# Performance work log

Measured on AMD Instinct MI355X. Metric: run time of the kernel, lower is better.

The kernel has to match this reference:

```python
import jax, jax.numpy as jnp
import numpy as np

N_NODES = 100000


def gcn_conv(x, edge_index, W, b):
    """PyG GCNConv: h = x @ W; out = D^-1/2 (A+I) D^-1/2 h + b."""
    n = x.shape[0]
    src, dst = edge_index[0], edge_index[1]
    loop = jnp.arange(n)
    src = jnp.concatenate([src, loop])  # add self-loops
    dst = jnp.concatenate([dst, loop])
    # degree at target nodes (unit edge weights)
    deg = jax.ops.segment_sum(jnp.ones(dst.shape[0], dtype=x.dtype), dst, num_segments=n)
    dinv = jnp.where(deg > 0, jax.lax.rsqrt(deg), 0.0)
    norm = dinv[src] * dinv[dst]  # [E+n]
    h = x @ W  # [n, out]
    msg = h[src] * norm[:, None]  # gather + scale
    out = jax.ops.segment_sum(msg, dst, num_segments=n)  # scatter-add
    return out + b


def setup_inputs() -> dict:
    key = jax.random.key(0)
    k1, k2, k3, k4, k5, k6 = jax.random.split(key, 6)
    E = 3200000
    x = jax.random.normal(k1, (N_NODES, 2), dtype=jnp.float32)
    edge_index = jax.random.randint(k2, (2, E), 0, N_NODES, dtype=jnp.int64)
    W1 = jax.random.normal(k3, (2, 16), dtype=jnp.float32) * 0.5
    b1 = jax.random.normal(k4, (16,), dtype=jnp.float32) * 0.1
    W2 = jax.random.normal(k5, (16, 2), dtype=jnp.float32) * 0.25
    b2 = jax.random.normal(k6, (2,), dtype=jnp.float32) * 0.1
    return {"x": x, "edge_index": edge_index, "W1": W1, "b1": b1, "W2": W2, "b2": b2}


def reference(x, edge_index, W1, b1, W2, b2):
    h = jax.nn.relu(gcn_conv(x, edge_index, W1, b1))
    # dropout is identity at inference
    out = gcn_conv(h, edge_index, W2, b2)
    return jax.nn.log_softmax(out, axis=1)
```

## Files before the change

### kernel.cpp

```cpp
#include <hip/hip_runtime.h>
#include <math.h>


constexpr int N = 100000;
constexpr int LOGB = 6;
constexpr int BNODES = 1 << LOGB;
constexpr int K = (N + BNODES - 1) / BNODES;
constexpr int KF = 49 * 32;
constexpr int CAPF = 2560;
constexpr int NC = 49;
constexpr int CAP1 = 68608;
constexpr int BSP = 512;
constexpr int ECHUNK = 8192;
constexpr int EPT = ECHUNK / BSP;
constexpr int MAXCH = 9;
constexpr int BAGG = 256;

__global__ __launch_bounds__(BSP) void k_pass1(const int* __restrict__ src,
                                               const int* __restrict__ dst, int E,
                                               int* __restrict__ gfill1,
                                               int* __restrict__ slotsC) {
    __shared__ int hist[NC];
    __shared__ int base[NC];
    int t = threadIdx.x;
    if (t < NC) hist[t] = 0;
    __syncthreads();
    int s[EPT], d[EPT];
    int ebase = blockIdx.x * ECHUNK + t * EPT;
#pragma unroll
    for (int k = 0; k < EPT / 4; k++) {
        int idx = ebase + 4 * k;
        if (idx + 3 < E) {
            *(int4*)(s + 4 * k) = *(const int4*)(src + idx);
            *(int4*)(d + 4 * k) = *(const int4*)(dst + idx);
        } else {
            for (int j = 0; j < 4; j++) {
                s[4 * k + j] = (idx + j < E) ? src[idx + j] : -1;
                d[4 * k + j] = (idx + j < E) ? dst[idx + j] : -1;
            }
        }
    }
#pragma unroll
    for (int k = 0; k < EPT; k++)
        if (d[k] >= 0) atomicAdd(&hist[d[k] >> 11], 1);
    __syncthreads();
    if (t < NC) {
        int c = hist[t];
        base[t] = c ? atomicAdd(&gfill1[t], c) : 0;
        hist[t] = 0;
    }
    __syncthreads();
#pragma unroll
    for (int k = 0; k < EPT; k++) {
        if (d[k] >= 0) {
            int bin = d[k] >> 11;
            int r = atomicAdd(&hist[bin], 1);
            int pos = base[bin] + r;
            if (pos < CAP1) slotsC[bin * CAP1 + pos] = (s[k] << 11) | (d[k] & 2047);
        }
    }
}

__global__ __launch_bounds__(BSP) void k_pass2(const int* __restrict__ gfill1,
                                               const int* __restrict__ slotsC,
                                               int* __restrict__ gfillF,
                                               int* __restrict__ slotsF,
                                               int* __restrict__ degPart) {
    __shared__ int hist[32];
    __shared__ int base[32];
    __shared__ int dh[2048];
    int c = blockIdx.x / MAXCH;
    int j = blockIdx.x % MAXCH;
    int fill = min(gfill1[c], CAP1);
    int e0 = j * ECHUNK;
    int t = threadIdx.x;
    int* dpRow = degPart + blockIdx.x * 2048;
    if (e0 >= fill) {
        for (int i = t; i < 2048; i += BSP) dpRow[i] = 0;
        return;
    }
    int e1 = min(fill, e0 + ECHUNK);
    if (t < 32) hist[t] = 0;
    for (int i = t; i < 2048; i += BSP) dh[i] = 0;
    __syncthreads();
    const int* row = slotsC + c * CAP1;
    int v[EPT];
    int ebase = e0 + t * EPT;
#pragma unroll
    for (int k = 0; k < EPT / 4; k++) {
        int idx = ebase + 4 * k;
        if (idx + 3 < e1) {
            *(int4*)(v + 4 * k) = *(const int4*)(row + idx);
        } else {
            for (int jj = 0; jj < 4; jj++) v[4 * k + jj] = (idx + jj < e1) ? row[idx + jj] : -1;
        }
    }
#pragma unroll
    for (int k = 0; k < EPT; k++)
        if (v[k] >= 0) {
            atomicAdd(&hist[(v[k] >> 6) & 31], 1);
            atomicAdd(&dh[v[k] & 2047], 1);
        }
    __syncthreads();
    if (t < 32) {
        int cc = hist[t];
        base[t] = cc ? atomicAdd(&gfillF[c * 32 + t], cc) : 0;
        hist[t] = 0;
    }
    __syncthreads();
#pragma unroll
    for (int k = 0; k < EPT; k++) {
        if (v[k] >= 0) {
            int b = (v[k] >> 6) & 31;
            int r = atomicAdd(&hist[b], 1);
            int pos = base[b] + r;
            if (pos < CAPF)
                slotsF[(c * 32 + b) * CAPF + pos] = ((v[k] >> 11) << 6) | (v[k] & 63);
        }
    }
    for (int i = t; i < 2048; i += BSP) dpRow[i] = dh[i];
}

__global__ __launch_bounds__(BAGG) void k_dinv(const int* __restrict__ degPart,
                                               const float* __restrict__ x,
                                               float* __restrict__ dinv,
                                               float2* __restrict__ sx) {
    int node = blockIdx.x * BAGG + threadIdx.x;
    if (node >= N) return;
    int c = node >> 11, i = node & 2047;
    const int* p = degPart + (size_t)c * MAXCH * 2048 + i;
    int deg = 0;
#pragma unroll
    for (int j = 0; j < MAXCH; j++) deg += p[j * 2048];
    float di = rsqrtf((float)(deg + 1));
    dinv[node] = di;
    float2 xv = ((const float2*)x)[node];
    sx[node] = make_float2(xv.x * di, xv.y * di);
}

__global__ __launch_bounds__(BAGG) void k_agg1(const int* __restrict__ gfillF,
                                               const int* __restrict__ slotsF,
                                               const float* __restrict__ dinv,
                                               const float2* __restrict__ sx,
                                               const float* __restrict__ W1,
                                               const float* __restrict__ b1,
                                               const float* __restrict__ W2,
                                               float2* __restrict__ sz) {
    __shared__ float accX[BNODES], accY[BNODES];
    __shared__ float sW1[32], sb1[16], sW2[32];
    int t = threadIdx.x;
    if (t < 32) sW1[t] = W1[t];
    if (t >= 32 && t < 48) sb1[t - 32] = b1[t - 32];
    if (t >= 48 && t < 80) sW2[t - 48] = W2[t - 48];
    if (t < BNODES) { accX[t] = 0.f; accY[t] = 0.f; }
    __syncthreads();
    int b = blockIdx.x;
    int count = min(gfillF[b], CAPF);
    const int* row = slotsF + b * CAPF;
    int nvec = count & ~3;
    for (int j = 4 * t; j < nvec; j += 4 * BAGG) {
        int4 p = *(const int4*)(row + j);
        float2 v0 = sx[p.x >> LOGB], v1 = sx[p.y >> LOGB];
        float2 v2 = sx[p.z >> LOGB], v3 = sx[p.w >> LOGB];
        atomicAdd(&accX[p.x & (BNODES - 1)], v0.x);
        atomicAdd(&accY[p.x & (BNODES - 1)], v0.y);
        atomicAdd(&accX[p.y & (BNODES - 1)], v1.x);
        atomicAdd(&accY[p.y & (BNODES - 1)], v1.y);
        atomicAdd(&accX[p.z & (BNODES - 1)], v2.x);
        atomicAdd(&accY[p.z & (BNODES - 1)], v2.y);
        atomicAdd(&accX[p.w & (BNODES - 1)], v3.x);
        atomicAdd(&accY[p.w & (BNODES - 1)], v3.y);
    }
    for (int j = nvec + t; j < count; j += BAGG) {
        int p = row[j];
        float2 v = sx[p >> LOGB];
        atomicAdd(&accX[p & (BNODES - 1)], v.x);
        atomicAdd(&accY[p & (BNODES - 1)], v.y);
    }
    __syncthreads();
    if (t < BNODES) {
        int node = b * BNODES + t;
        if (node < N) {
            float di = dinv[node];
            float2 sv = sx[node];
            float a0 = (accX[t] + sv.x) * di;
            float a1 = (accY[t] + sv.y) * di;
            float z0 = 0.f, z1 = 0.f;
#pragma unroll
            for (int k = 0; k < 16; k++) {
                float h = fmaf(a0, sW1[k], fmaf(a1, sW1[16 + k], sb1[k]));
                h = fmaxf(h, 0.f);
                z0 = fmaf(h, sW2[2 * k + 0], z0);
                z1 = fmaf(h, sW2[2 * k + 1], z1);
            }
            sz[node] = make_float2(z0 * di, z1 * di);
        }
    }
}

__global__ __launch_bounds__(BAGG) void k_agg2(const int* __restrict__ gfillF,
                                               const int* __restrict__ slotsF,
                                               const float* __restrict__ dinv,
                                               const float2* __restrict__ sz,
                                               const float* __restrict__ b2,
                                               float2* __restrict__ out) {
    __shared__ float accX[BNODES], accY[BNODES];
    int b = blockIdx.x, t = threadIdx.x;
    if (t < BNODES) { accX[t] = 0.f; accY[t] = 0.f; }
    __syncthreads();
    int count = min(gfillF[b], CAPF);
    const int* row = slotsF + b * CAPF;
    int nvec = count & ~3;
    for (int j = 4 * t; j < nvec; j += 4 * BAGG) {
        int4 p = *(const int4*)(row + j);
        float2 v0 = sz[p.x >> LOGB], v1 = sz[p.y >> LOGB];
        float2 v2 = sz[p.z >> LOGB], v3 = sz[p.w >> LOGB];
        atomicAdd(&accX[p.x & (BNODES - 1)], v0.x);
        atomicAdd(&accY[p.x & (BNODES - 1)], v0.y);
        atomicAdd(&accX[p.y & (BNODES - 1)], v1.x);
        atomicAdd(&accY[p.y & (BNODES - 1)], v1.y);
        atomicAdd(&accX[p.z & (BNODES - 1)], v2.x);
        atomicAdd(&accY[p.z & (BNODES - 1)], v2.y);
        atomicAdd(&accX[p.w & (BNODES - 1)], v3.x);
        atomicAdd(&accY[p.w & (BNODES - 1)], v3.y);
    }
    for (int j = nvec + t; j < count; j += BAGG) {
        int p = row[j];
        float2 v = sz[p >> LOGB];
        atomicAdd(&accX[p & (BNODES - 1)], v.x);
        atomicAdd(&accY[p & (BNODES - 1)], v.y);
    }
    __syncthreads();
    if (t < BNODES) {
        int node = b * BNODES + t;
        if (node < N) {
            float di = dinv[node];
            float2 sv = sz[node];
            float v0 = fmaf(accX[t] + sv.x, di, b2[0]);
            float v1 = fmaf(accY[t] + sv.y, di, b2[1]);
            float m = fmaxf(v0, v1);
            float lse = m + logf(expf(v0 - m) + expf(v1 - m));
            out[node] = make_float2(v0 - lse, v1 - lse);
        }
    }
}

extern "C" void kernel_launch(void* const* d_in, const int* in_sizes, int n_in,
                              void* d_out, int out_size, void* d_ws, size_t ws_size,
                              hipStream_t stream) {
    const float* x  = (const float*)d_in[0];
    const int*   ei = (const int*)d_in[1];
    const float* W1 = (const float*)d_in[2];
    const float* b1 = (const float*)d_in[3];
    const float* W2 = (const float*)d_in[4];
    const float* b2 = (const float*)d_in[5];

    const int E = in_sizes[1] / 2;
    const int* src = ei;
    const int* dst = ei + E;
    const int GP = (E + ECHUNK - 1) / ECHUNK;

    char* ws = (char*)d_ws;
    size_t off = 0;
    auto alloc = [&](size_t bytes) {
        char* p = ws + off;
        off += (bytes + 511) & ~size_t(511);
        return p;
    };
    int*    fills   = (int*)alloc((NC + KF) * sizeof(int));
    float*  dinv    = (float*)alloc(N * sizeof(float));
    float2* sx      = (float2*)alloc(N * sizeof(float2));
    float2* sz      = (float2*)alloc(N * sizeof(float2));
    int*    slotsC  = (int*)alloc((size_t)NC * CAP1 * sizeof(int));
    int*    slotsF  = (int*)alloc((size_t)KF * CAPF * sizeof(int));
    int*    degPart = (int*)alloc((size_t)NC * MAXCH * 2048 * sizeof(int));
    int* gfill1 = fills;
    int* gfillF = fills + NC;

    hipMemsetAsync(fills, 0, (NC + KF) * sizeof(int), stream);

    k_pass1<<<GP, BSP, 0, stream>>>(src, dst, E, gfill1, slotsC);
    k_pass2<<<NC * MAXCH, BSP, 0, stream>>>(gfill1, slotsC, gfillF, slotsF, degPart);
    k_dinv<<<(N + BAGG - 1) / BAGG, BAGG, 0, stream>>>(degPart, x, dinv, sx);
    k_agg1<<<K, BAGG, 0, stream>>>(gfillF, slotsF, dinv, sx, W1, b1, W2, sz);
    k_agg2<<<K, BAGG, 0, stream>>>(gfillF, slotsF, dinv, sz, b2, (float2*)d_out);
}
```

Before: 199.6 us.

## Drop fine binning; aggregate from coarse bins with per-chunk partial sums

Removes the second binning pass that built 64-node fine bins, and aggregates directly from the 2048-node coarse bins. Each block accumulates into a 2048-entry shared-memory array and writes per-chunk partial sums, which separate per-node combine kernels reduce and finish with the dense transform or log-softmax. This cuts the slotsF scatter writes and the atomics needed to build them. In exchange it adds two more kernel launches and partial-sum global traffic, and places more atomic traffic on a larger shared array.

```diff
diff --git a/kernel.cpp b/kernel.cpp
--- a/kernel.cpp
+++ b/kernel.cpp
@@ -3,18 +3,13 @@
 
 
 constexpr int N = 100000;
-constexpr int LOGB = 6;
-constexpr int BNODES = 1 << LOGB;
-constexpr int K = (N + BNODES - 1) / BNODES;
-constexpr int KF = 49 * 32;
-constexpr int CAPF = 2560;
 constexpr int NC = 49;
+constexpr int CB = 2048;
 constexpr int CAP1 = 68608;
 constexpr int BSP = 512;
 constexpr int ECHUNK = 8192;
 constexpr int EPT = ECHUNK / BSP;
 constexpr int MAXCH = 9;
-constexpr int BAGG = 256;
 
 __global__ __launch_bounds__(BSP) void k_pass1(const int* __restrict__ src,
                                                const int* __restrict__ dst, int E,
@@ -61,27 +56,17 @@
     }
 }
 
-__global__ __launch_bounds__(BSP) void k_pass2(const int* __restrict__ gfill1,
-                                               const int* __restrict__ slotsC,
-                                               int* __restrict__ gfillF,
-                                               int* __restrict__ slotsF,
-                                               int* __restrict__ degPart) {
-    __shared__ int hist[32];
-    __shared__ int base[32];
-    __shared__ int dh[2048];
-    int c = blockIdx.x / MAXCH;
-    int j = blockIdx.x % MAXCH;
+__global__ __launch_bounds__(BSP) void k_deg(const int* __restrict__ gfill1,
+                                             const int* __restrict__ slotsC,
+                                             int* __restrict__ degPart) {
+    __shared__ int dh[CB];
+    int c = blockIdx.x / MAXCH, j = blockIdx.x % MAXCH;
     int fill = min(gfill1[c], CAP1);
     int e0 = j * ECHUNK;
-    int t = threadIdx.x;
-    int* dpRow = degPart + blockIdx.x * 2048;
-    if (e0 >= fill) {
-        for (int i = t; i < 2048; i += BSP) dpRow[i] = 0;
-        return;
-    }
+    if (e0 >= fill) return;
     int e1 = min(fill, e0 + ECHUNK);
-    if (t < 32) hist[t] = 0;
-    for (int i = t; i < 2048; i += BSP) dh[i] = 0;
+    int t = threadIdx.x;
+    for (int i = t; i < CB; i += BSP) dh[i] = 0;
     __syncthreads();
     const int* row = slotsC + c * CAP1;
     int v[EPT];
@@ -97,152 +82,133 @@
     }
 #pragma unroll
     for (int k = 0; k < EPT; k++)
-        if (v[k] >= 0) {
-            atomicAdd(&hist[(v[k] >> 6) & 31], 1);
-            atomicAdd(&dh[v[k] & 2047], 1);
-        }
-    __syncthreads();
-    if (t < 32) {
-        int cc = hist[t];
-        base[t] = cc ? atomicAdd(&gfillF[c * 32 + t], cc) : 0;
-        hist[t] = 0;
-    }
-    __syncthreads();
-#pragma unroll
-    for (int k = 0; k < EPT; k++) {
-        if (v[k] >= 0) {
-            int b = (v[k] >> 6) & 31;
-            int r = atomicAdd(&hist[b], 1);
-            int pos = base[b] + r;
-            if (pos < CAPF)
-                slotsF[(c * 32 + b) * CAPF + pos] = ((v[k] >> 11) << 6) | (v[k] & 63);
-        }
-    }
-    for (int i = t; i < 2048; i += BSP) dpRow[i] = dh[i];
-}
-
-__global__ __launch_bounds__(BAGG) void k_dinv(const int* __restrict__ degPart,
-                                               const float* __restrict__ x,
-                                               float* __restrict__ dinv,
-                                               float2* __restrict__ sx) {
-    int node = blockIdx.x * BAGG + threadIdx.x;
+        if (v[k] >= 0) atomicAdd(&dh[v[k] & (CB - 1)], 1);
+    __syncthreads();
+    int* dp = degPart + blockIdx.x * CB;
+    for (int i = t; i < CB; i += BSP) dp[i] = dh[i];
+}
+
+__global__ __launch_bounds__(256) void k_dinv(const int* __restrict__ gfill1,
+                                              const int* __restrict__ degPart,
+                                              const float* __restrict__ x,
+                                              float* __restrict__ dinv,
+                                              float2* __restrict__ sx) {
+    int node = blockIdx.x * 256 + threadIdx.x;
     if (node >= N) return;
-    int c = node >> 11, i = node & 2047;
-    const int* p = degPart + (size_t)c * MAXCH * 2048 + i;
+    int c = node >> 11, i = node & (CB - 1);
+    int nch = (min(gfill1[c], CAP1) + ECHUNK - 1) / ECHUNK;
+    const int* p = degPart + c * MAXCH * CB + i;
     int deg = 0;
-#pragma unroll
-    for (int j = 0; j < MAXCH; j++) deg += p[j * 2048];
+    for (int j = 0; j < nch; j++) deg += p[j * CB];
     float di = rsqrtf((float)(deg + 1));
     dinv[node] = di;
     float2 xv = ((const float2*)x)[node];
     sx[node] = make_float2(xv.x * di, xv.y * di);
 }
 
-__global__ __launch_bounds__(BAGG) void k_agg1(const int* __restrict__ gfillF,
-                                               const int* __restrict__ slotsF,
+__global__ __launch_bounds__(BSP) void k_aggc(const int* __restrict__ gfill1,
+                                              const int* __restrict__ slotsC,
+                                              const float2* __restrict__ vals,
+                                              float* __restrict__ partX,
+                                              float* __restrict__ partY) {
+    __shared__ float aX[CB], aY[CB];
+    int c = blockIdx.x / MAXCH, j = blockIdx.x % MAXCH;
+    int fill = min(gfill1[c], CAP1);
+    int e0 = j * ECHUNK;
+    if (e0 >= fill) return;
+    int e1 = min(fill, e0 + ECHUNK);
+    int t = threadIdx.x;
+    for (int i = t; i < CB; i += BSP) { aX[i] = 0.f; aY[i] = 0.f; }
+    __syncthreads();
+    const int* row = slotsC + c * CAP1;
+    int v[EPT];
+    int ebase = e0 + t * EPT;
+#pragma unroll
+    for (int k = 0; k < EPT / 4; k++) {
+        int idx = ebase + 4 * k;
+        if (idx + 3 < e1) {
+            *(int4*)(v + 4 * k) = *(const int4*)(row + idx);
+        } else {
+            for (int jj = 0; jj < 4; jj++) v[4 * k + jj] = (idx + jj < e1) ? row[idx + jj] : -1;
+        }
+    }
+    float2 g[EPT];
+#pragma unroll
+    for (int k = 0; k < EPT; k++) g[k] = (v[k] >= 0) ? vals[v[k] >> 11] : make_float2(0.f, 0.f);
+#pragma unroll
+    for (int k = 0; k < EPT; k++) {
+        if (v[k] >= 0) {
+            int d = v[k] & (CB - 1);
+            atomicAdd(&aX[d], g[k].x);
+            atomicAdd(&aY[d], g[k].y);
+        }
+    }
+    __syncthreads();
+    float* px = partX + blockIdx.x * CB;
+    float* py = partY + blockIdx.x * CB;
+    for (int i = t; i < CB; i += BSP) { px[i] = aX[i]; py[i] = aY[i]; }
+}
+
+__global__ __launch_bounds__(256) void k_comb1(const int* __restrict__ gfill1,
+                                               const float* __restrict__ partX,
+                                               const float* __restrict__ partY,
                                                const float* __restrict__ dinv,
                                                const float2* __restrict__ sx,
                                                const float* __restrict__ W1,
                                                const float* __restrict__ b1,
                                                const float* __restrict__ W2,
                                                float2* __restrict__ sz) {
-    __shared__ float accX[BNODES], accY[BNODES];
     __shared__ float sW1[32], sb1[16], sW2[32];
     int t = threadIdx.x;
     if (t < 32) sW1[t] = W1[t];
-    if (t >= 32 && t < 48) sb1[t - 32] = b1[t - 32];
-    if (t >= 48 && t < 80) sW2[t - 48] = W2[t - 48];
-    if (t < BNODES) { accX[t] = 0.f; accY[t] = 0.f; }
-    __syncthreads();
-    int b = blockIdx.x;
-    int count = min(gfillF[b], CAPF);
-    const int* row = slotsF + b * CAPF;
-    int nvec = count & ~3;
-    for (int j = 4 * t; j < nvec; j += 4 * BAGG) {
-        int4 p = *(const int4*)(row + j);
-        float2 v0 = sx[p.x >> LOGB], v1 = sx[p.y >> LOGB];
-        float2 v2 = sx[p.z >> LOGB], v3 = sx[p.w >> LOGB];
-        atomicAdd(&accX[p.x & (BNODES - 1)], v0.x);
-        atomicAdd(&accY[p.x & (BNODES - 1)], v0.y);
-        atomicAdd(&accX[p.y & (BNODES - 1)], v1.x);
-        atomicAdd(&accY[p.y & (BNODES - 1)], v1.y);
-        atomicAdd(&accX[p.z & (BNODES - 1)], v2.x);
-        atomicAdd(&accY[p.z & (BNODES - 1)], v2.y);
-        atomicAdd(&accX[p.w & (BNODES - 1)], v3.x);
-        atomicAdd(&accY[p.w & (BNODES - 1)], v3.y);
-    }
-    for (int j = nvec + t; j < count; j += BAGG) {
-        int p = row[j];
-        float2 v = sx[p >> LOGB];
-        atomicAdd(&accX[p & (BNODES - 1)], v.x);
-        atomicAdd(&accY[p & (BNODES - 1)], v.y);
-    }
-    __syncthreads();
-    if (t < BNODES) {
-        int node = b * BNODES + t;
-        if (node < N) {
-            float di = dinv[node];
-            float2 sv = sx[node];
-            float a0 = (accX[t] + sv.x) * di;
-            float a1 = (accY[t] + sv.y) * di;
-            float z0 = 0.f, z1 = 0.f;
-#pragma unroll
-            for (int k = 0; k < 16; k++) {
-                float h = fmaf(a0, sW1[k], fmaf(a1, sW1[16 + k], sb1[k]));
-                h = fmaxf(h, 0.f);
-                z0 = fmaf(h, sW2[2 * k + 0], z0);
-                z1 = fmaf(h, sW2[2 * k + 1], z1);
-            }
-            sz[node] = make_float2(z0 * di, z1 * di);
-        }
-    }
-}
-
-__global__ __launch_bounds__(BAGG) void k_agg2(const int* __restrict__ gfillF,
-                                               const int* __restrict__ slotsF,
+    else if (t < 48) sb1[t - 32] = b1[t - 32];
+    else if (t < 80) sW2[t - 48] = W2[t - 48];
+    __syncthreads();
+    int node = blockIdx.x * 256 + t;
+    if (node >= N) return;
+    int c = node >> 11, i = node & (CB - 1);
+    int nch = (min(gfill1[c], CAP1) + ECHUNK - 1) / ECHUNK;
+    const float* px = partX + c * MAXCH * CB + i;
+    const float* py = partY + c * MAXCH * CB + i;
+    float ax = 0.f, ay = 0.f;
+    for (int j = 0; j < nch; j++) { ax += px[j * CB]; ay += py[j * CB]; }
+    float di = dinv[node];
+    float2 sv = sx[node];
+    float a0 = (ax + sv.x) * di;
+    float a1 = (ay + sv.y) * di;
+    float z0 = 0.f, z1 = 0.f;
+#pragma unroll
+    for (int k = 0; k < 16; k++) {
+        float h = fmaf(a0, sW1[k], fmaf(a1, sW1[16 + k], sb1[k]));
+        h = fmaxf(h, 0.f);
+        z0 = fmaf(h, sW2[2 * k + 0], z0);
+        z1 = fmaf(h, sW2[2 * k + 1], z1);
+    }
+    sz[node] = make_float2(z0 * di, z1 * di);
+}
+
+__global__ __launch_bounds__(256) void k_comb2(const int* __restrict__ gfill1,
+                                               const float* __restrict__ partX,
+                                               const float* __restrict__ partY,
                                                const float* __restrict__ dinv,
                                                const float2* __restrict__ sz,
                                                const float* __restrict__ b2,
                                                float2* __restrict__ out) {
-    __shared__ float accX[BNODES], accY[BNODES];
-    int b = blockIdx.x, t = threadIdx.x;
-    if (t < BNODES) { accX[t] = 0.f; accY[t] = 0.f; }
-    __syncthreads();
-    int count = min(gfillF[b], CAPF);
-    const int* row = slotsF + b * CAPF;
-    int nvec = count & ~3;
-    for (int j = 4 * t; j < nvec; j += 4 * BAGG) {
-        int4 p = *(const int4*)(row + j);
-        float2 v0 = sz[p.x >> LOGB], v1 = sz[p.y >> LOGB];
-        float2 v2 = sz[p.z >> LOGB], v3 = sz[p.w >> LOGB];
-        atomicAdd(&accX[p.x & (BNODES - 1)], v0.x);
-        atomicAdd(&accY[p.x & (BNODES - 1)], v0.y);
-        atomicAdd(&accX[p.y & (BNODES - 1)], v1.x);
-        atomicAdd(&accY[p.y & (BNODES - 1)], v1.y);
-        atomicAdd(&accX[p.z & (BNODES - 1)], v2.x);
-        atomicAdd(&accY[p.z & (BNODES - 1)], v2.y);
-        atomicAdd(&accX[p.w & (BNODES - 1)], v3.x);
-        atomicAdd(&accY[p.w & (BNODES - 1)], v3.y);
-    }
-    for (int j = nvec + t; j < count; j += BAGG) {
-        int p = row[j];
-        float2 v = sz[p >> LOGB];
-        atomicAdd(&accX[p & (BNODES - 1)], v.x);
-        atomicAdd(&accY[p & (BNODES - 1)], v.y);
-    }
-    __syncthreads();
-    if (t < BNODES) {
-        int node = b * BNODES + t;
-        if (node < N) {
-            float di = dinv[node];
-            float2 sv = sz[node];
-            float v0 = fmaf(accX[t] + sv.x, di, b2[0]);
-            float v1 = fmaf(accY[t] + sv.y, di, b2[1]);
-            float m = fmaxf(v0, v1);
-            float lse = m + logf(expf(v0 - m) + expf(v1 - m));
-            out[node] = make_float2(v0 - lse, v1 - lse);
-        }
-    }
+    int node = blockIdx.x * 256 + threadIdx.x;
+    if (node >= N) return;
+    int c = node >> 11, i = node & (CB - 1);
+    int nch = (min(gfill1[c], CAP1) + ECHUNK - 1) / ECHUNK;
+    const float* px = partX + c * MAXCH * CB + i;
+    const float* py = partY + c * MAXCH * CB + i;
+    float ax = 0.f, ay = 0.f;
+    for (int j = 0; j < nch; j++) { ax += px[j * CB]; ay += py[j * CB]; }
+    float di = dinv[node];
+    float2 sv = sz[node];
+    float v0 = fmaf(ax + sv.x, di, b2[0]);
+    float v1 = fmaf(ay + sv.y, di, b2[1]);
+    float m = fmaxf(v0, v1);
+    float lse = m + logf(expf(v0 - m) + expf(v1 - m));
+    out[node] = make_float2(v0 - lse, v1 - lse);
 }
 
 extern "C" void kernel_launch(void* const* d_in, const int* in_sizes, int n_in,
@@ -259,6 +225,8 @@
     const int* src = ei;
     const int* dst = ei + E;
     const int GP = (E + ECHUNK - 1) / ECHUNK;
+    const int GB = NC * MAXCH;
+    const int GN = (N + 255) / 256;
 
     char* ws = (char*)d_ws;
     size_t off = 0;
@@ -267,21 +235,22 @@
         off += (bytes + 511) & ~size_t(511);
         return p;
     };
-    int*    fills   = (int*)alloc((NC + KF) * sizeof(int));
+    int*    gfill1  = (int*)alloc(NC * sizeof(int));
     float*  dinv    = (float*)alloc(N * sizeof(float));
     float2* sx      = (float2*)alloc(N * sizeof(float2));
     float2* sz      = (float2*)alloc(N * sizeof(float2));
     int*    slotsC  = (int*)alloc((size_t)NC * CAP1 * sizeof(int));
-    int*    slotsF  = (int*)alloc((size_t)KF * CAPF * sizeof(int));
-    int*    degPart = (int*)alloc((size_t)NC * MAXCH * 2048 * sizeof(int));
-    int* gfill1 = fills;
-    int* gfillF = fills + NC;
-
-    hipMemsetAsync(fills, 0, (NC + KF) * sizeof(int), stream);
+    int*    degPart = (int*)alloc((size_t)GB * CB * sizeof(int));
+    float*  partX   = (float*)alloc((size_t)GB * CB * sizeof(float));
+    float*  partY   = (float*)alloc((size_t)GB * CB * sizeof(float));
+
+    hipMemsetAsync(gfill1, 0, NC * sizeof(int), stream);
 
     k_pass1<<<GP, BSP, 0, stream>>>(src, dst, E, gfill1, slotsC);
-    k_pass2<<<NC * MAXCH, BSP, 0, stream>>>(gfill1, slotsC, gfillF, slotsF, degPart);
-    k_dinv<<<(N + BAGG - 1) / BAGG, BAGG, 0, stream>>>(degPart, x, dinv, sx);
-    k_agg1<<<K, BAGG, 0, stream>>>(gfillF, slotsF, dinv, sx, W1, b1, W2, sz);
-    k_agg2<<<K, BAGG, 0, stream>>>(gfillF, slotsF, dinv, sz, b2, (float2*)d_out);
-}
+    k_deg<<<GB, BSP, 0, stream>>>(gfill1, slotsC, degPart);
+    k_dinv<<<GN, 256, 0, stream>>>(gfill1, degPart, x, dinv, sx);
+    k_aggc<<<GB, BSP, 0, stream>>>(gfill1, slotsC, sx, partX, partY);
+    k_comb1<<<GN, 256, 0, stream>>>(gfill1, partX, partY, dinv, sx, W1, b1, W2, sz);
+    k_aggc<<<GB, BSP, 0, stream>>>(gfill1, slotsC, sz, partX, partY);
+    k_comb2<<<GN, 256, 0, stream>>>(gfill1, partX, partY, dinv, sz, b2, (float2*)d_out);
+}
```

Result: slower. 221.3 us (+10.9%).
